# Performance work log

Measured on AMD Instinct MI355X. Metric: run time of the kernel, lower is better.

## Reference

```python
import jax, jax.numpy as jnp
import numpy as np

GRID_SIZE = 5
SPLINE_ORDER = 3
N_COEFF = GRID_SIZE + SPLINE_ORDER  # 8 spline coefficients per edge
NUM_HEADS = 4


def make_grid():
    # grid on [-1, 1] extended by spline_order on each side (efficient-kan style)
    h = 2.0 / GRID_SIZE
    return jnp.arange(-SPLINE_ORDER, GRID_SIZE + SPLINE_ORDER + 1, dtype=jnp.float32) * h - 1.0


def b_splines(x, grid):
    # x: [N, in] -> bases: [N, in, N_COEFF] via Cox-de Boor recursion
    xe = x[..., None]
    bases = ((xe >= grid[:-1]) & (xe < grid[1:])).astype(x.dtype)
    for j in range(1, SPLINE_ORDER + 1):
        bases = ((xe - grid[:-(j + 1)]) / (grid[j:-1] - grid[:-(j + 1)]) * bases[..., :-1]
                 + (grid[j + 1:] - xe) / (grid[j + 1:] - grid[1:-j]) * bases[..., 1:])
    return bases


def kan_linear(x, base_w, spline_w, grid):
    # base branch: silu(x) @ W_base^T ; spline branch: sum_c B_c(x_i) * W_spline[o,i,c]
    return jax.nn.silu(x) @ base_w.T + jnp.einsum('nic,oic->no', b_splines(x, grid), spline_w)


def setup_inputs() -> dict:
    key = jax.random.key(0)
    ks = jax.random.split(key, 16)
    D, Hd, B, S = 512, 1024, 8, 1024
    def bw(k, o, i):
        return jax.random.normal(k, (o, i), jnp.float32) * (1.0 / np.sqrt(i))
    def sw(k, o, i):
        return jax.random.normal(k, (o, i, N_COEFF), jnp.float32) * 0.1
    return {
        'x': jax.random.normal(ks[0], (B, S, D), jnp.float32),
        'k1_base': bw(ks[1], Hd, D), 'k1_spline': sw(ks[2], Hd, D),
        'k2_base': bw(ks[3], D, Hd), 'k2_spline': sw(ks[4], D, Hd),
        'q_base': bw(ks[5], D, D), 'q_spline': sw(ks[6], D, D),
        'k_base': bw(ks[7], D, D), 'k_spline': sw(ks[8], D, D),
        'v_base': bw(ks[9], D, D), 'v_spline': sw(ks[10], D, D),
        'o_base': bw(ks[11], D, D), 'o_spline': sw(ks[12], D, D),
        'ln_w': jnp.ones((D,), jnp.float32),
        'ln_b': jnp.zeros((D,), jnp.float32),
    }


def reference(x, k1_base, k1_spline, k2_base, k2_spline,
              q_base, q_spline, k_base, k_spline, v_base, v_spline,
              o_base, o_spline, ln_w, ln_b):
    grid = make_grid()
    B, S, D = x.shape
    xf = x.reshape(-1, D)
    # KAN1 -> ReLU -> KAN2
    h = jax.nn.relu(kan_linear(xf, k1_base, k1_spline, grid))
    h = kan_linear(h, k2_base, k2_spline, grid)  # [B*S, D]
    # AttKAN: KAN projections + multi-head self-attention + KAN output proj
    q = kan_linear(h, q_base, q_spline, grid)
    k = kan_linear(h, k_base, k_spline, grid)
    v = kan_linear(h, v_base, v_spline, grid)
    dh = D // NUM_HEADS
    def split(t):
        return t.reshape(B, S, NUM_HEADS, dh).transpose(0, 2, 1, 3)  # [B,H,S,dh]
    qh, kh, vh = split(q), split(k), split(v)
    attn = jax.nn.softmax(jnp.einsum('bhqd,bhkd->bhqk', qh, kh) / np.sqrt(dh).astype(np.float32), axis=-1)
    o = jnp.einsum('bhqk,bhkd->bhqd', attn, vh).transpose(0, 2, 1, 3).reshape(-1, D)
    o = kan_linear(o, o_base, o_spline, grid)
    # dropout is identity in eval; residual + LayerNorm
    out = o.reshape(B, S, D) + x
    mu = out.mean(-1, keepdims=True)
    var = out.var(-1, keepdims=True)
    return (out - mu) / jnp.sqrt(var + 1e-5) * ln_w + ln_b
```

## Files before the change

kernel.cpp:

```cpp
#include <hip/hip_runtime.h>
#include <cstdint>

typedef unsigned short ushort_t;
typedef _Float16 half_t;
typedef __attribute__((ext_vector_type(8))) short short8;
typedef __attribute__((ext_vector_type(8))) half_t half8;
typedef __attribute__((ext_vector_type(4))) half_t half4;
typedef __attribute__((ext_vector_type(4))) float f32x4;

__device__ __forceinline__ void gld_lds16(const ushort_t* g, ushort_t* l) {
    __builtin_amdgcn_global_load_lds((const __attribute__((address_space(1))) void*)g,
                                     (__attribute__((address_space(3))) void*)l,
                                     16, 0, 0);
}

template<int IN>
__global__ void expand_kernel(const float* __restrict__ X, half_t* __restrict__ E, int nrows) {
    int idx = blockIdx.x * 256 + threadIdx.x;
    if (idx >= nrows * IN) return;
    int n = idx / IN, i = idx % IN;
    float x = X[idx];
    float si = x / (1.0f + __expf(-x));
    float u = (x + 2.2f) * 2.5f;
    int ji = (int)floorf(u);
    float f = u - (float)ji;
    if (!(ji >= 0 && ji <= 10)) ji = -100;
    float f2 = f * f, f3 = f2 * f;
    float w_i   = f3 * (1.0f / 6.0f);
    float w_im1 = (1.0f + 3.0f * f + 3.0f * f2 - 3.0f * f3) * (1.0f/6.0f);
    float w_im2 = (4.0f - 6.0f * f2 + 3.0f * f3) * (1.0f/6.0f);
    float omf = 1.0f - f;
    float w_im3 = omf * omf * omf * (1.0f / 6.0f);
    half_t* Er = E + (long)n * 9 * IN + i;
    Er[0] = (half_t)si;
    #pragma unroll
    for (int c = 0; c < 8; ++c) {
        float v = 0.0f;
        v = (c == ji    ) ? w_i   : v;
        v = (c == ji - 1) ? w_im1 : v;
        v = (c == ji - 2) ? w_im2 : v;
        v = (c == ji - 3) ? w_im3 : v;
        Er[(long)(c + 1) * IN] = (half_t)v;
    }
}

template<int IN>
__global__ void pack_kernel(const float* __restrict__ base, const float* __restrict__ spline,
                            half_t* __restrict__ Whi, half_t* __restrict__ Wlo, int nout) {
    int idx = blockIdx.x * 256 + threadIdx.x;
    if (idx >= nout * IN) return;
    int o = idx / IN, i = idx % IN;
    long r0 = (long)o * 9 * IN + i;
    float w[9];
    w[0] = base[idx];
    const f32x4* sp = (const f32x4*)(spline + (long)idx * 8);
    f32x4 s0 = sp[0], s1 = sp[1];
    w[1] = s0[0]; w[2] = s0[1]; w[3] = s0[2]; w[4] = s0[3];
    w[5] = s1[0]; w[6] = s1[1]; w[7] = s1[2]; w[8] = s1[3];
    #pragma unroll
    for (int c = 0; c < 9; ++c) {
        half_t hi = (half_t)w[c];
        half_t lo = (half_t)(w[c] - (float)hi);
        Whi[r0 + (long)c * IN] = hi;
        Wlo[r0 + (long)c * IN] = lo;
    }
}

enum { EPI_PART = 0, EPI_QKV = 1, EPI_SH = 2, EPI_PV = 3, EPI_RELU = 4 };

template<int EPI, int NPASS, int KSPLIT>
__global__ __launch_bounds__(256, 4)
void gemm_w(const ushort_t* __restrict__ A, const ushort_t* __restrict__ Bhi,
            const ushort_t* __restrict__ Blo, float* __restrict__ Cf, float* __restrict__ P,
            half_t* __restrict__ Qp, half_t* __restrict__ Kp, half_t* __restrict__ Vp,
            int M, int N, int K) {
    __shared__ __attribute__((aligned(16))) ushort_t As[128 * 64];
    __shared__ __attribute__((aligned(16))) ushort_t Bs[128 * 64];
    const int tid = threadIdx.x;
    const int lane = tid & 63;
    const int wave = tid >> 6;
    const int wm = wave >> 1, wn = wave & 1;
    const int bm = blockIdx.x * 128, bn = blockIdx.y * 128;
    const int l15 = lane & 15, l16 = lane >> 4;
    const int NT = K >> 6;
    const int TV = (NPASS == 2) ? 2 * NT : NT;
    int kc, t0;
    if constexpr (KSPLIT > 1) { kc = TV / KSPLIT; t0 = blockIdx.z * kc; }
    else { kc = TV; t0 = 0; }

    f32x4 acc[4][4];
    #pragma unroll
    for (int m = 0; m < 4; ++m)
        #pragma unroll
        for (int n = 0; n < 4; ++n) acc[m][n] = (f32x4){0.f, 0.f, 0.f, 0.f};

    for (int u = 0; u < kc; ++u) {
        int tt = t0 + u;
        int pass = (tt >= NT) ? 1 : 0;
        int kt = (tt - (pass ? NT : 0)) << 6;
        const ushort_t* Bb = pass ? Blo : Bhi;
        #pragma unroll
        for (int r = 0; r < 4; ++r) {
            int ch = r * 256 + tid;
            int row = ch >> 3, c = ch & 7;
            gld_lds16(A + (long)(bm + row) * K + kt + ((c ^ (row & 7)) << 3), &As[ch * 8]);
        }
        #pragma unroll
        for (int r = 0; r < 4; ++r) {
            int ch = r * 256 + tid;
            int row = ch >> 3, c = ch & 7;
            gld_lds16(Bb + (long)(bn + row) * K + kt + ((c ^ (row & 7)) << 3), &Bs[ch * 8]);
        }
        __syncthreads();
        #pragma unroll
        for (int kk = 0; kk < 2; ++kk) {
            half8 af[4], bfr[4];
            #pragma unroll
            for (int m = 0; m < 4; ++m) {
                int row = wm * 64 + m * 16 + l15;
                af[m] = __builtin_bit_cast(half8, *(const short8*)&As[row * 64 + (((kk * 4 + l16) ^ (row & 7)) << 3)]);
            }
            #pragma unroll
            for (int n = 0; n < 4; ++n) {
                int row = wn * 64 + n * 16 + l15;
                bfr[n] = __builtin_bit_cast(half8, *(const short8*)&Bs[row * 64 + (((kk * 4 + l16) ^ (row & 7)) << 3)]);
            }
            #pragma unroll
            for (int m = 0; m < 4; ++m)
                #pragma unroll
                for (int n = 0; n < 4; ++n)
                    acc[m][n] = __builtin_amdgcn_mfma_f32_16x16x32_f16(af[m], bfr[n], acc[m][n], 0, 0, 0);
        }
        __syncthreads();
    }

    #pragma unroll
    for (int m = 0; m < 4; ++m) {
        #pragma unroll
        for (int n = 0; n < 4; ++n) {
            #pragma unroll
            for (int j = 0; j < 4; ++j) {
                int row = bm + wm * 64 + m * 16 + l16 * 4 + j;
                int col = bn + wn * 64 + n * 16 + l15;
                float v = acc[m][n][j];
                if constexpr (KSPLIT > 1) {
                    P[(size_t)blockIdx.z * M * N + (long)row * N + col] = v;
                } else if constexpr (EPI == EPI_RELU) {
                    Cf[(long)row * N + col] = fmaxf(v, 0.0f);
                } else if constexpr (EPI == EPI_QKV) {
                    int which = col >> 9, w5 = col & 511, h = w5 >> 7, d = w5 & 127;
                    int b = row >> 10, ss = row & 1023;
                    half_t* dst = (which == 0) ? Qp : ((which == 1) ? Kp : Vp);
                    dst[(((long)(b * 4 + h) * 1024 + ss) << 7) + d] = (half_t)v;
                }
            }
        }
    }
}

template<int EPI>
__global__ void gemm_t(const ushort_t* __restrict__ A, const ushort_t* __restrict__ B,
                       float* __restrict__ Cf, half_t* __restrict__ Sh,
                       int M, int N, int K, long sA, long sB, long sC, float scale) {
    __shared__ ushort_t As[128 * 64];
    __shared__ ushort_t Bs[128 * 64];
    const int tid = threadIdx.x;
    const int lane = tid & 63;
    const int wave = tid >> 6;
    const int wm = wave >> 1, wn = wave & 1;
    const int bm = blockIdx.x * 128, bn = blockIdx.y * 128;
    const int z = blockIdx.z;
    const int l15 = lane & 15, l16 = lane >> 4;
    const ushort_t* Ab = A + (long)z * sA;
    const ushort_t* Bb = B + (long)z * sB;

    f32x4 acc[4][4];
    #pragma unroll
    for (int m = 0; m < 4; ++m)
        #pragma unroll
        for (int n = 0; n < 4; ++n) acc[m][n] = (f32x4){0.f, 0.f, 0.f, 0.f};

    for (int kt = 0; kt < K; kt += 64) {
        #pragma unroll
        for (int r = 0; r < 4; ++r) {
            int chunk = r * 256 + tid;
            gld_lds16(Ab + (long)(bm + (chunk >> 3)) * K + kt + ((chunk & 7) << 3), &As[chunk * 8]);
        }
        #pragma unroll
        for (int r = 0; r < 4; ++r) {
            int chunk = r * 256 + tid;
            gld_lds16(Bb + (long)(bn + (chunk >> 3)) * K + kt + ((chunk & 7) << 3), &Bs[chunk * 8]);
        }
        __syncthreads();
        #pragma unroll
        for (int kk = 0; kk < 2; ++kk) {
            half8 af[4], bfr[4];
            #pragma unroll
            for (int m = 0; m < 4; ++m)
                af[m] = __builtin_bit_cast(half8, *(const short8*)&As[(wm * 64 + m * 16 + l15) * 64 + kk * 32 + l16 * 8]);
            #pragma unroll
            for (int n = 0; n < 4; ++n)
                bfr[n] = __builtin_bit_cast(half8, *(const short8*)&Bs[(wn * 64 + n * 16 + l15) * 64 + kk * 32 + l16 * 8]);
            #pragma unroll
            for (int m = 0; m < 4; ++m)
                #pragma unroll
                for (int n = 0; n < 4; ++n)
                    acc[m][n] = __builtin_amdgcn_mfma_f32_16x16x32_f16(af[m], bfr[n], acc[m][n], 0, 0, 0);
        }
        __syncthreads();
    }

    #pragma unroll
    for (int m = 0; m < 4; ++m) {
        #pragma unroll
        for (int n = 0; n < 4; ++n) {
            #pragma unroll
            for (int j = 0; j < 4; ++j) {
                int row = bm + wm * 64 + m * 16 + l16 * 4 + j;
                int col = bn + wn * 64 + n * 16 + l15;
                float v = acc[m][n][j];
                if constexpr (EPI == EPI_SH) {
                    Sh[(long)z * sC + (long)row * N + col] = (half_t)(v * scale);
                } else if constexpr (EPI == EPI_PV) {
                    int b = z >> 2, h = z & 3;
                    Cf[((long)(b * 1024 + row) * 512) + h * 128 + col] = v;
                }
            }
        }
    }
}

template<int KS, bool RELU>
__global__ void reduce_kernel(const float* __restrict__ P, float* __restrict__ out, long MN) {
    long i = ((long)blockIdx.x * 256 + threadIdx.x) * 4;
    if (i >= MN) return;
    f32x4 s = *(const f32x4*)&P[i];
    #pragma unroll
    for (int zz = 1; zz < KS; ++zz) {
        f32x4 t = *(const f32x4*)&P[(size_t)zz * MN + i];
        s += t;
    }
    if constexpr (RELU) {
        s[0] = fmaxf(s[0], 0.f); s[1] = fmaxf(s[1], 0.f);
        s[2] = fmaxf(s[2], 0.f); s[3] = fmaxf(s[3], 0.f);
    }
    *(f32x4*)&out[i] = s;
}

__global__ void transpose_v(const ushort_t* __restrict__ V, ushort_t* __restrict__ Vt) {
    __shared__ ushort_t t[64][72];
    int s0 = blockIdx.x * 64, d0 = blockIdx.y * 64, bh = blockIdx.z;
    const ushort_t* Vb = V + (long)bh * 1024 * 128;
    ushort_t* Vtb = Vt + (long)bh * 128 * 1024;
    int tid = threadIdx.x;
    int r = tid >> 2, g = tid & 3;
    #pragma unroll
    for (int j = 0; j < 16; ++j)
        t[r][g * 16 + j] = Vb[(long)(s0 + r) * 128 + d0 + g * 16 + j];
    __syncthreads();
    #pragma unroll
    for (int j = 0; j < 16; ++j)
        Vtb[(long)(d0 + r) * 1024 + s0 + g * 16 + j] = t[g * 16 + j][r];
}

__global__ void softmax_kernel(const half_t* __restrict__ S, half_t* __restrict__ P) {
    long row = (long)blockIdx.x * 4 + (threadIdx.x >> 6);
    int lane = threadIdx.x & 63;
    const half_t* Sr = S + row * 1024;
    float f[16];
    #pragma unroll
    for (int c = 0; c < 2; ++c) {
        half8 h = *(const half8*)&Sr[c * 512 + lane * 8];
        #pragma unroll
        for (int j = 0; j < 8; ++j) f[c * 8 + j] = (float)h[j];
    }
    float mx = -3.0e38f;
    #pragma unroll
    for (int j = 0; j < 16; ++j) mx = fmaxf(mx, f[j]);
    #pragma unroll
    for (int off = 32; off > 0; off >>= 1) mx = fmaxf(mx, __shfl_xor(mx, off));
    float sum = 0.0f;
    #pragma unroll
    for (int j = 0; j < 16; ++j) { f[j] = __expf(f[j] - mx); sum += f[j]; }
    #pragma unroll
    for (int off = 32; off > 0; off >>= 1) sum += __shfl_xor(sum, off);
    float inv = 1.0f / sum;
    half_t* Pr = P + row * 1024;
    #pragma unroll
    for (int c = 0; c < 2; ++c) {
        half8 o;
        #pragma unroll
        for (int j = 0; j < 8; ++j) o[j] = (half_t)(f[c * 8 + j] * inv);
        *(half8*)&Pr[c * 512 + lane * 8] = o;
    }
}

__global__ void reduce2_ln_kernel(const float* __restrict__ P, long MN,
                                  const float* __restrict__ X,
                                  const float* __restrict__ g, const float* __restrict__ b,
                                  float* __restrict__ out) {
    long row = (long)blockIdx.x * 4 + (threadIdx.x >> 6);
    int lane = threadIdx.x & 63;
    long base = row * 512 + lane * 8;
    f32x4 p0 = *(const f32x4*)&P[base],      p1 = *(const f32x4*)&P[base + 4];
    f32x4 q0 = *(const f32x4*)&P[MN + base], q1 = *(const f32x4*)&P[MN + base + 4];
    f32x4 x0 = *(const f32x4*)&X[base],      x1 = *(const f32x4*)&X[base + 4];
    float y[8];
    #pragma unroll
    for (int j = 0; j < 4; ++j) {
        y[j]     = (p0[j] + q0[j]) + x0[j];
        y[j + 4] = (p1[j] + q1[j]) + x1[j];
    }
    float s = 0.f;
    #pragma unroll
    for (int j = 0; j < 8; ++j) s += y[j];
    #pragma unroll
    for (int off = 32; off > 0; off >>= 1) s += __shfl_xor(s, off);
    float mu = s * (1.0f / 512.0f);
    float vs = 0.f;
    #pragma unroll
    for (int j = 0; j < 8; ++j) { float d = y[j] - mu; vs += d * d; }
    #pragma unroll
    for (int off = 32; off > 0; off >>= 1) vs += __shfl_xor(vs, off);
    float r = rsqrtf(vs * (1.0f / 512.0f) + 1e-5f);
    f32x4 w0 = *(const f32x4*)&g[lane * 8], w1 = *(const f32x4*)&g[lane * 8 + 4];
    f32x4 b0 = *(const f32x4*)&b[lane * 8], b1 = *(const f32x4*)&b[lane * 8 + 4];
    f32x4 r0, r1;
    #pragma unroll
    for (int j = 0; j < 4; ++j) {
        r0[j] = (y[j] - mu) * r * w0[j] + b0[j];
        r1[j] = (y[j + 4] - mu) * r * w1[j] + b1[j];
    }
    *(f32x4*)&out[base] = r0;
    *(f32x4*)&out[base + 4] = r1;
}

extern "C" void kernel_launch(void* const* d_in, const int* in_sizes, int n_in,
                              void* d_out, int out_size, void* d_ws, size_t ws_size,
                              hipStream_t stream) {
    const float* x         = (const float*)d_in[0];
    const float* k1_base   = (const float*)d_in[1];
    const float* k1_spline = (const float*)d_in[2];
    const float* k2_base   = (const float*)d_in[3];
    const float* k2_spline = (const float*)d_in[4];
    const float* q_base    = (const float*)d_in[5];
    const float* q_spline  = (const float*)d_in[6];
    const float* k_base    = (const float*)d_in[7];
    const float* k_spline  = (const float*)d_in[8];
    const float* v_base    = (const float*)d_in[9];
    const float* v_spline  = (const float*)d_in[10];
    const float* o_base    = (const float*)d_in[11];
    const float* o_spline  = (const float*)d_in[12];
    const float* ln_w      = (const float*)d_in[13];
    const float* ln_b      = (const float*)d_in[14];
    float* out = (float*)d_out;

    constexpr int Dm = 512, HD = 1024, NR = 8192;
    constexpr int K1 = 9 * Dm;
    constexpr int K2 = 9 * HD;
    constexpr long SQ = (long)1024 * 128;
    constexpr long SS = (long)1024 * 1024;
    constexpr size_t MB = 1024 * 1024;

    char* p = (char*)d_ws;
    size_t off = 0;
    auto take = [&](size_t bytes) -> char* {
        char* r = p + off;
        off += (bytes + 255) & ~(size_t)255;
        return r;
    };
    half_t* W1hi = (half_t*)take((size_t)HD * K1 * 2);
    half_t* W2hi = (half_t*)take((size_t)Dm * K2 * 2);
    half_t* Wqhi = (half_t*)take((size_t)3 * Dm * K1 * 2);
    half_t* Wohi = (half_t*)take((size_t)Dm * K1 * 2);
    half_t* W1lo = (half_t*)take((size_t)HD * K1 * 2);
    half_t* W2lo = (half_t*)take((size_t)Dm * K2 * 2);
    half_t* Wqlo = (half_t*)take((size_t)3 * Dm * K1 * 2);
    half_t* Wolo = (half_t*)take((size_t)Dm * K1 * 2);
    char*   A    = take((size_t)152 * MB);
    (void)ws_size; (void)in_sizes; (void)n_in; (void)out_size;

    half_t* E1   = (half_t*)(A);
    float*  H1   = (float*)(A + 72 * MB);
    half_t* E2   = (half_t*)(A);
    float*  P2   = (float*)(A + 104 * MB);
    float*  H2   = (float*)(A + 136 * MB);
    half_t* E3   = (half_t*)(A);
    half_t* Qb   = (half_t*)(A + 72 * MB);
    half_t* Kb   = (half_t*)(A + 80 * MB);
    half_t* Vb   = (half_t*)(A + 88 * MB);
    half_t* Vt   = (half_t*)(A + 96 * MB);
    half_t* Schk = (half_t*)(A);
    float*  AO   = (float*)(A + 104 * MB);
    half_t* E4   = (half_t*)(A);
    float*  P3   = (float*)(A + 120 * MB);

    pack_kernel<Dm><<<(HD * Dm) / 256, 256, 0, stream>>>(k1_base, k1_spline, W1hi, W1lo, HD);
    pack_kernel<HD><<<(Dm * HD) / 256, 256, 0, stream>>>(k2_base, k2_spline, W2hi, W2lo, Dm);
    pack_kernel<Dm><<<(Dm * Dm) / 256, 256, 0, stream>>>(q_base, q_spline, Wqhi, Wqlo, Dm);
    pack_kernel<Dm><<<(Dm * Dm) / 256, 256, 0, stream>>>(k_base, k_spline, Wqhi + (size_t)Dm * K1, Wqlo + (size_t)Dm * K1, Dm);
    pack_kernel<Dm><<<(Dm * Dm) / 256, 256, 0, stream>>>(v_base, v_spline, Wqhi + (size_t)2 * Dm * K1, Wqlo + (size_t)2 * Dm * K1, Dm);
    pack_kernel<Dm><<<(Dm * Dm) / 256, 256, 0, stream>>>(o_base, o_spline, Wohi, Wolo, Dm);

    expand_kernel<Dm><<<(NR * Dm) / 256, 256, 0, stream>>>(x, E1, NR);
    gemm_w<EPI_RELU, 2, 1><<<dim3(NR / 128, HD / 128, 1), 256, 0, stream>>>(
        (const ushort_t*)E1, (const ushort_t*)W1hi, (const ushort_t*)W1lo,
        H1, nullptr, nullptr, nullptr, nullptr, NR, HD, K1);

    for (int c = 0; c < 2; ++c) {
        expand_kernel<HD><<<(4096 * HD) / 256, 256, 0, stream>>>(H1 + (size_t)c * 4096 * HD, E2, 4096);
        gemm_w<EPI_PART, 2, 4><<<dim3(4096 / 128, Dm / 128, 4), 256, 0, stream>>>(
            (const ushort_t*)E2, (const ushort_t*)W2hi, (const ushort_t*)W2lo,
            nullptr, P2, nullptr, nullptr, nullptr, 4096, Dm, K2);
        reduce_kernel<4, false><<<(4096 * Dm) / 1024, 256, 0, stream>>>(P2, H2 + (size_t)c * 4096 * Dm, (long)4096 * Dm);
    }

    expand_kernel<Dm><<<(NR * Dm) / 256, 256, 0, stream>>>(H2, E3, NR);
    gemm_w<EPI_QKV, 1, 1><<<dim3(NR / 128, (3 * Dm) / 128, 1), 256, 0, stream>>>(
        (const ushort_t*)E3, (const ushort_t*)Wqhi, (const ushort_t*)Wqlo,
        nullptr, nullptr, Qb, Kb, Vb, NR, 3 * Dm, K1);

    transpose_v<<<dim3(16, 2, 32), 256, 0, stream>>>((const ushort_t*)Vb, (ushort_t*)Vt);
    gemm_t<EPI_SH><<<dim3(8, 8, 32), 256, 0, stream>>>(
        (const ushort_t*)Qb, (const ushort_t*)Kb,
        nullptr, Schk, 1024, 1024, 128, SQ, SQ, SS, 0.08838834764831845f);
    softmax_kernel<<<(32 * 1024) / 4, 256, 0, stream>>>(Schk, Schk);
    gemm_t<EPI_PV><<<dim3(8, 1, 32), 256, 0, stream>>>(
        (const ushort_t*)Schk, (const ushort_t*)Vt, AO, nullptr,
        1024, 128, 1024, SS, SQ, 0, 1.f);

    expand_kernel<Dm><<<(NR * Dm) / 256, 256, 0, stream>>>(AO, E4, NR);
    gemm_w<EPI_PART, 1, 2><<<dim3(NR / 128, Dm / 128, 2), 256, 0, stream>>>(
        (const ushort_t*)E4, (const ushort_t*)Wohi, (const ushort_t*)Wolo,
        nullptr, P3, nullptr, nullptr, nullptr, NR, Dm, K1);
    reduce2_ln_kernel<<<NR / 4, 256, 0, stream>>>(P3, (long)NR * Dm, x, ln_w, ln_b, out);
}
```

Before: 717.8 us.

## Fuse QK^T, softmax and PV into a single flash-attention kernel

Replaces the separate score GEMM, softmax kernel and PV GEMM with one fused kernel using online softmax. Q tiles stay in registers, while K, V and P tiles are staged in XOR-swizzled shared memory. This removes the writing and re-reading of the full fp16 score matrix in global memory and two kernel launches. In exchange, each block holds 128KB of LDS and runs at one block per CU, with no overlap between loads and compute.

```diff
diff --git a/kernel.cpp b/kernel.cpp
--- a/kernel.cpp
+++ b/kernel.cpp
@@ -5,7 +5,6 @@
 typedef _Float16 half_t;
 typedef __attribute__((ext_vector_type(8))) short short8;
 typedef __attribute__((ext_vector_type(8))) half_t half8;
-typedef __attribute__((ext_vector_type(4))) half_t half4;
 typedef __attribute__((ext_vector_type(4))) float f32x4;
 
 __device__ __forceinline__ void gld_lds16(const ushort_t* g, ushort_t* l) {
@@ -66,7 +65,7 @@
     }
 }
 
-enum { EPI_PART = 0, EPI_QKV = 1, EPI_SH = 2, EPI_PV = 3, EPI_RELU = 4 };
+enum { EPI_PART = 0, EPI_QKV = 1, EPI_RELU = 4 };
 
 template<int EPI, int NPASS, int KSPLIT>
 __global__ __launch_bounds__(256, 4)
@@ -158,73 +157,151 @@
     }
 }
 
-template<int EPI>
-__global__ void gemm_t(const ushort_t* __restrict__ A, const ushort_t* __restrict__ B,
-                       float* __restrict__ Cf, half_t* __restrict__ Sh,
-                       int M, int N, int K, long sA, long sB, long sC, float scale) {
-    __shared__ ushort_t As[128 * 64];
-    __shared__ ushort_t Bs[128 * 64];
+__global__ __launch_bounds__(256, 1)
+void flash_attn(const ushort_t* __restrict__ Q, const ushort_t* __restrict__ Kb,
+                const ushort_t* __restrict__ Vt, float* __restrict__ AO, float scale) {
+    constexpr int TS = 128 * 128;
+    __shared__ __attribute__((aligned(16))) ushort_t Qs[TS];
+    __shared__ __attribute__((aligned(16))) ushort_t Ks[TS];
+    __shared__ __attribute__((aligned(16))) ushort_t Vs[TS];
+    __shared__ __attribute__((aligned(16))) half_t  Ps[TS];
     const int tid = threadIdx.x;
     const int lane = tid & 63;
-    const int wave = tid >> 6;
-    const int wm = wave >> 1, wn = wave & 1;
-    const int bm = blockIdx.x * 128, bn = blockIdx.y * 128;
-    const int z = blockIdx.z;
+    const int w = tid >> 6;
     const int l15 = lane & 15, l16 = lane >> 4;
-    const ushort_t* Ab = A + (long)z * sA;
-    const ushort_t* Bb = B + (long)z * sB;
-
-    f32x4 acc[4][4];
-    #pragma unroll
-    for (int m = 0; m < 4; ++m)
-        #pragma unroll
-        for (int n = 0; n < 4; ++n) acc[m][n] = (f32x4){0.f, 0.f, 0.f, 0.f};
-
-    for (int kt = 0; kt < K; kt += 64) {
-        #pragma unroll
-        for (int r = 0; r < 4; ++r) {
-            int chunk = r * 256 + tid;
-            gld_lds16(Ab + (long)(bm + (chunk >> 3)) * K + kt + ((chunk & 7) << 3), &As[chunk * 8]);
-        }
-        #pragma unroll
-        for (int r = 0; r < 4; ++r) {
-            int chunk = r * 256 + tid;
-            gld_lds16(Bb + (long)(bn + (chunk >> 3)) * K + kt + ((chunk & 7) << 3), &Bs[chunk * 8]);
+    const int bm = blockIdx.x * 128;
+    const int bh = blockIdx.y;
+    const ushort_t* Qg = Q + (long)bh * 1024 * 128;
+    const ushort_t* Kg = Kb + (long)bh * 1024 * 128;
+    const ushort_t* Vg = Vt + (long)bh * 128 * 1024;
+
+    #pragma unroll
+    for (int r = 0; r < 8; ++r) {
+        int ch = r * 256 + tid;
+        int row = ch >> 4, c = ch & 15;
+        gld_lds16(Qg + (long)(bm + row) * 128 + ((c ^ (row & 15)) << 3), &Qs[ch * 8]);
+    }
+    __syncthreads();
+    half8 qf[2][4];
+    #pragma unroll
+    for (int mf = 0; mf < 2; ++mf)
+        #pragma unroll
+        for (int kk = 0; kk < 4; ++kk) {
+            int row = w * 32 + mf * 16 + l15;
+            qf[mf][kk] = __builtin_bit_cast(half8, *(const short8*)&Qs[row * 128 + (((kk * 4 + l16) ^ (row & 15)) << 3)]);
+        }
+
+    f32x4 o_acc[2][8];
+    #pragma unroll
+    for (int mf = 0; mf < 2; ++mf)
+        #pragma unroll
+        for (int nf = 0; nf < 8; ++nf) o_acc[mf][nf] = (f32x4){0.f, 0.f, 0.f, 0.f};
+    float m_run[2][4], l_run[2][4];
+    #pragma unroll
+    for (int mf = 0; mf < 2; ++mf)
+        #pragma unroll
+        for (int j = 0; j < 4; ++j) { m_run[mf][j] = -3.0e38f; l_run[mf][j] = 0.f; }
+
+    for (int t = 0; t < 8; ++t) {
+        int kv0 = t * 128;
+        #pragma unroll
+        for (int r = 0; r < 8; ++r) {
+            int ch = r * 256 + tid;
+            int row = ch >> 4, c = ch & 15;
+            gld_lds16(Kg + (long)(kv0 + row) * 128 + ((c ^ (row & 15)) << 3), &Ks[ch * 8]);
+        }
+        #pragma unroll
+        for (int r = 0; r < 8; ++r) {
+            int ch = r * 256 + tid;
+            int row = ch >> 4, c = ch & 15;
+            gld_lds16(Vg + (long)row * 1024 + kv0 + ((c ^ (row & 15)) << 3), (ushort_t*)&Vs[ch * 8]);
         }
         __syncthreads();
-        #pragma unroll
-        for (int kk = 0; kk < 2; ++kk) {
-            half8 af[4], bfr[4];
-            #pragma unroll
-            for (int m = 0; m < 4; ++m)
-                af[m] = __builtin_bit_cast(half8, *(const short8*)&As[(wm * 64 + m * 16 + l15) * 64 + kk * 32 + l16 * 8]);
-            #pragma unroll
-            for (int n = 0; n < 4; ++n)
-                bfr[n] = __builtin_bit_cast(half8, *(const short8*)&Bs[(wn * 64 + n * 16 + l15) * 64 + kk * 32 + l16 * 8]);
-            #pragma unroll
-            for (int m = 0; m < 4; ++m)
-                #pragma unroll
-                for (int n = 0; n < 4; ++n)
-                    acc[m][n] = __builtin_amdgcn_mfma_f32_16x16x32_f16(af[m], bfr[n], acc[m][n], 0, 0, 0);
-        }
+        f32x4 s_acc[2][8];
+        #pragma unroll
+        for (int mf = 0; mf < 2; ++mf)
+            #pragma unroll
+            for (int nf = 0; nf < 8; ++nf) s_acc[mf][nf] = (f32x4){0.f, 0.f, 0.f, 0.f};
+        #pragma unroll
+        for (int nf = 0; nf < 8; ++nf) {
+            #pragma unroll
+            for (int kk = 0; kk < 4; ++kk) {
+                int row = nf * 16 + l15;
+                half8 bf = __builtin_bit_cast(half8, *(const short8*)&Ks[row * 128 + (((kk * 4 + l16) ^ (row & 15)) << 3)]);
+                #pragma unroll
+                for (int mf = 0; mf < 2; ++mf)
+                    s_acc[mf][nf] = __builtin_amdgcn_mfma_f32_16x16x32_f16(qf[mf][kk], bf, s_acc[mf][nf], 0, 0, 0);
+            }
+        }
+        #pragma unroll
+        for (int mf = 0; mf < 2; ++mf) {
+            #pragma unroll
+            for (int j = 0; j < 4; ++j) {
+                float rmax = -3.0e38f;
+                #pragma unroll
+                for (int nf = 0; nf < 8; ++nf) rmax = fmaxf(rmax, s_acc[mf][nf][j]);
+                #pragma unroll
+                for (int off = 1; off < 16; off <<= 1) rmax = fmaxf(rmax, __shfl_xor(rmax, off));
+                float m_new = fmaxf(m_run[mf][j], rmax * scale);
+                float alpha = __expf(m_run[mf][j] - m_new);
+                m_run[mf][j] = m_new;
+                float rsum = 0.f;
+                #pragma unroll
+                for (int nf = 0; nf < 8; ++nf) {
+                    float pv = __expf(s_acc[mf][nf][j] * scale - m_new);
+                    s_acc[mf][nf][j] = pv;
+                    rsum += pv;
+                }
+                #pragma unroll
+                for (int off = 1; off < 16; off <<= 1) rsum += __shfl_xor(rsum, off);
+                l_run[mf][j] = l_run[mf][j] * alpha + rsum;
+                #pragma unroll
+                for (int nf = 0; nf < 8; ++nf) o_acc[mf][nf][j] *= alpha;
+            }
+        }
+        #pragma unroll
+        for (int mf = 0; mf < 2; ++mf)
+            #pragma unroll
+            for (int nf = 0; nf < 8; ++nf)
+                #pragma unroll
+                for (int j = 0; j < 4; ++j) {
+                    int row = w * 32 + mf * 16 + l16 * 4 + j;
+                    int col = nf * 16 + l15;
+                    int sch = (col >> 3) ^ (row & 15);
+                    Ps[row * 128 + (sch << 3) + (col & 7)] = (half_t)s_acc[mf][nf][j];
+                }
         __syncthreads();
-    }
-
-    #pragma unroll
-    for (int m = 0; m < 4; ++m) {
-        #pragma unroll
-        for (int n = 0; n < 4; ++n) {
+        half8 pf[2][4];
+        #pragma unroll
+        for (int mf = 0; mf < 2; ++mf)
+            #pragma unroll
+            for (int kk = 0; kk < 4; ++kk) {
+                int row = w * 32 + mf * 16 + l15;
+                pf[mf][kk] = __builtin_bit_cast(half8, *(const short8*)&Ps[row * 128 + (((kk * 4 + l16) ^ (row & 15)) << 3)]);
+            }
+        #pragma unroll
+        for (int nf = 0; nf < 8; ++nf) {
+            #pragma unroll
+            for (int kk = 0; kk < 4; ++kk) {
+                int row = nf * 16 + l15;
+                half8 bf = __builtin_bit_cast(half8, *(const short8*)&Vs[row * 128 + (((kk * 4 + l16) ^ (row & 15)) << 3)]);
+                #pragma unroll
+                for (int mf = 0; mf < 2; ++mf)
+                    o_acc[mf][nf] = __builtin_amdgcn_mfma_f32_16x16x32_f16(pf[mf][kk], bf, o_acc[mf][nf], 0, 0, 0);
+            }
+        }
+        __syncthreads();
+    }
+    int b = bh >> 2, h = bh & 3;
+    #pragma unroll
+    for (int mf = 0; mf < 2; ++mf) {
+        #pragma unroll
+        for (int nf = 0; nf < 8; ++nf) {
             #pragma unroll
             for (int j = 0; j < 4; ++j) {
-                int row = bm + wm * 64 + m * 16 + l16 * 4 + j;
-                int col = bn + wn * 64 + n * 16 + l15;
-                float v = acc[m][n][j];
-                if constexpr (EPI == EPI_SH) {
-                    Sh[(long)z * sC + (long)row * N + col] = (half_t)(v * scale);
-                } else if constexpr (EPI == EPI_PV) {
-                    int b = z >> 2, h = z & 3;
-                    Cf[((long)(b * 1024 + row) * 512) + h * 128 + col] = v;
-                }
+                int row = bm + w * 32 + mf * 16 + l16 * 4 + j;
+                int col = nf * 16 + l15;
+                AO[(long)(b * 1024 + row) * 512 + h * 128 + col] = o_acc[mf][nf][j] / l_run[mf][j];
             }
         }
     }
@@ -261,38 +338,6 @@
     #pragma unroll
     for (int j = 0; j < 16; ++j)
         Vtb[(long)(d0 + r) * 1024 + s0 + g * 16 + j] = t[g * 16 + j][r];
-}
-
-__global__ void softmax_kernel(const half_t* __restrict__ S, half_t* __restrict__ P) {
-    long row = (long)blockIdx.x * 4 + (threadIdx.x >> 6);
-    int lane = threadIdx.x & 63;
-    const half_t* Sr = S + row * 1024;
-    float f[16];
-    #pragma unroll
-    for (int c = 0; c < 2; ++c) {
-        half8 h = *(const half8*)&Sr[c * 512 + lane * 8];
-        #pragma unroll
-        for (int j = 0; j < 8; ++j) f[c * 8 + j] = (float)h[j];
-    }
-    float mx = -3.0e38f;
-    #pragma unroll
-    for (int j = 0; j < 16; ++j) mx = fmaxf(mx, f[j]);
-    #pragma unroll
-    for (int off = 32; off > 0; off >>= 1) mx = fmaxf(mx, __shfl_xor(mx, off));
-    float sum = 0.0f;
-    #pragma unroll
-    for (int j = 0; j < 16; ++j) { f[j] = __expf(f[j] - mx); sum += f[j]; }
-    #pragma unroll
-    for (int off = 32; off > 0; off >>= 1) sum += __shfl_xor(sum, off);
-    float inv = 1.0f / sum;
-    half_t* Pr = P + row * 1024;
-    #pragma unroll
-    for (int c = 0; c < 2; ++c) {
-        half8 o;
-        #pragma unroll
-        for (int j = 0; j < 8; ++j) o[j] = (half_t)(f[c * 8 + j] * inv);
-        *(half8*)&Pr[c * 512 + lane * 8] = o;
-    }
 }
 
 __global__ void reduce2_ln_kernel(const float* __restrict__ P, long MN,
@@ -358,8 +403,6 @@
     constexpr int Dm = 512, HD = 1024, NR = 8192;
     constexpr int K1 = 9 * Dm;
     constexpr int K2 = 9 * HD;
-    constexpr long SQ = (long)1024 * 128;
-    constexpr long SS = (long)1024 * 1024;
     constexpr size_t MB = 1024 * 1024;
 
     char* p = (char*)d_ws;
@@ -390,7 +433,6 @@
     half_t* Kb   = (half_t*)(A + 80 * MB);
     half_t* Vb   = (half_t*)(A + 88 * MB);
     half_t* Vt   = (half_t*)(A + 96 * MB);
-    half_t* Schk = (half_t*)(A);
     float*  AO   = (float*)(A + 104 * MB);
     half_t* E4   = (half_t*)(A);
     float*  P3   = (float*)(A + 120 * MB);
@@ -421,13 +463,9 @@
         nullptr, nullptr, Qb, Kb, Vb, NR, 3 * Dm, K1);
 
     transpose_v<<<dim3(16, 2, 32), 256, 0, stream>>>((const ushort_t*)Vb, (ushort_t*)Vt);
-    gemm_t<EPI_SH><<<dim3(8, 8, 32), 256, 0, stream>>>(
-        (const ushort_t*)Qb, (const ushort_t*)Kb,
-        nullptr, Schk, 1024, 1024, 128, SQ, SQ, SS, 0.08838834764831845f);
-    softmax_kernel<<<(32 * 1024) / 4, 256, 0, stream>>>(Schk, Schk);
-    gemm_t<EPI_PV><<<dim3(8, 1, 32), 256, 0, stream>>>(
-        (const ushort_t*)Schk, (const ushort_t*)Vt, AO, nullptr,
-        1024, 128, 1024, SS, SQ, 0, 1.f);
+    flash_attn<<<dim3(8, 32), 256, 0, stream>>>(
+        (const ushort_t*)Qb, (const ushort_t*)Kb, (const ushort_t*)Vt, AO,
+        0.08838834764831845f);
 
     expand_kernel<Dm><<<(NR * Dm) / 256, 256, 0, stream>>>(AO, E4, NR);
     gemm_w<EPI_PART, 1, 2><<<dim3(NR / 128, Dm / 128, 2), 256, 0, stream>>>(
```

Result: no change. 712.8 us (-0.7%).
